# Kernel optimization log

Hardware: AMD Instinct MI355X
Metric: run time of the kernel (lower is better)

Reference implementation:

```python
import jax, jax.numpy as jnp
import numpy as np

B, LQ, LK, E, HID, H = 4, 1024, 2048, 512, 512, 8


def _ln(x, g, b, eps=1e-5):
    mu = jnp.mean(x, -1, keepdims=True)
    var = jnp.mean((x - mu) ** 2, -1, keepdims=True)
    return (x - mu) * jax.lax.rsqrt(var + eps) * g + b


def _mha(q_in, k_in, v_in, Wq, bq, Wk, bk, Wv, bv, Wo, bo, nheads, q_valid, k_valid):
    # torch nn.MultiheadAttention (batch_first, eval/dropout=0) math
    Bq, Lq, Em = q_in.shape
    Lk = k_in.shape[1]
    hd = Em // nheads
    q = (q_in @ Wq.T + bq).reshape(Bq, Lq, nheads, hd)
    k = (k_in @ Wk.T + bk).reshape(Bq, Lk, nheads, hd)
    v = (v_in @ Wv.T + bv).reshape(Bq, Lk, nheads, hd)
    scale = 1.0 / np.sqrt(hd).astype(np.float32)
    s = jnp.einsum('bqhd,bkhd->bhqk', q, k) * scale
    if k_valid is not None:
        # valid query rows may only attend to valid key columns
        s = jnp.where(k_valid[:, None, None, :], s, jnp.finfo(s.dtype).min)
    w = jax.nn.softmax(s, axis=-1)
    # rows beyond a sample's length are fully masked in the torch nested path
    # (softmax -> NaN, later nan_to_num'd to 0); we zero them directly.
    w = jnp.where(q_valid[:, None, :, None], w, 0.0)
    o = jnp.einsum('bhqk,bkhd->bqhd', w, v).reshape(Bq, Lq, Em)
    return o @ Wo.T + bo, jnp.mean(w, axis=1)  # weights averaged over heads


def setup_inputs() -> dict:
    key = jax.random.key(0)
    ks = jax.random.split(key, 32)
    p = lambda i, shape: 0.02 * jax.random.normal(ks[i], shape, dtype=jnp.float32)
    inp = {
        'queries': jax.random.normal(ks[0], (B, LQ, E), dtype=jnp.float32),
        'keys': jax.random.normal(ks[1], (B, LK, E), dtype=jnp.float32),
        'q_len': jax.random.randint(ks[2], (B,), 1, LQ + 1),
        # cross-attention params
        'cWq': p(3, (E, E)), 'cbq': jnp.zeros((E,)),
        'cWk': p(4, (E, E)), 'cbk': jnp.zeros((E,)),
        'cWv': p(5, (E, E)), 'cbv': jnp.zeros((E,)),
        'cWo': p(6, (E, E)), 'cbo': jnp.zeros((E,)),
        # self-attention params
        'sWq': p(7, (HID, HID)), 'sbq': jnp.zeros((HID,)),
        'sWk': p(8, (HID, HID)), 'sbk': jnp.zeros((HID,)),
        'sWv': p(9, (HID, HID)), 'sbv': jnp.zeros((HID,)),
        'sWo': p(10, (HID, HID)), 'sbo': jnp.zeros((HID,)),
        # ffn + norms
        'Wf': p(11, (HID, E)), 'bf': jnp.zeros((HID,)),
        'g_cross': jnp.ones((E,)), 'b_cross': jnp.zeros((E,)),
        'g_ffn': jnp.ones((HID,)), 'b_ffn': jnp.zeros((HID,)),
        'g_self': jnp.ones((HID,)), 'b_self': jnp.zeros((HID,)),
    }
    return inp


def reference(queries, keys, q_len,
              cWq, cbq, cWk, cbk, cWv, cbv, cWo, cbo,
              sWq, sbq, sWk, sbk, sWv, sbv, sWo, sbo,
              Wf, bf, g_cross, b_cross, g_ffn, b_ffn, g_self, b_self):
    valid = jnp.arange(LQ)[None, :] < q_len[:, None]  # [B, LQ] ragged lengths
    q = jnp.where(valid[..., None], queries, 0.0)     # nested -> padded with 0
    # cross attention: valid rows attend to ALL keys (per the nested mask)
    cross, weights = _mha(q, keys, keys, cWq, cbq, cWk, cbk, cWv, cbv, cWo, cbo,
                          H, valid, None)
    q = _ln(jax.nn.silu(cross + q), g_cross, b_cross)
    f = q @ Wf.T + bf
    q = _ln(jax.nn.silu(q + f), g_ffn, b_ffn)  # q_dim == hidden_dim branch
    q = jnp.where(valid[..., None], q, 0.0)    # torch.nan_to_num on padded rows
    # self attention: valid rows attend only to valid rows of the same sample
    so, _ = _mha(q, q, q, sWq, sbq, sWk, sbk, sWv, sbv, sWo, sbo, H, valid, valid)
    q = _ln(jax.nn.silu(q + so), g_self, b_self)
    q = jnp.where(valid[..., None], q, 0.0)    # padded rows discarded by unbind
    return q, weights
```

## Files before the change

kernel.cpp:

```cpp
#include <hip/hip_runtime.h>

#define BB 4
#define SLQ 1024
#define SLK 2048
#define EE 512
#define HH 8
#define HD 64

typedef unsigned short u16;
typedef __attribute__((ext_vector_type(8))) short s16x8;
typedef __attribute__((ext_vector_type(4))) float f32x4;

__device__ __forceinline__ float bf2f(u16 u) {
  union { unsigned int i; float f; } v; v.i = ((unsigned int)u) << 16; return v.f;
}
__device__ __forceinline__ u16 f2bf(float f) {
  union { float f; unsigned int i; } v; v.f = f;
  unsigned int i = v.i;
  return (u16)((i + 0x7fffu + ((i >> 16) & 1u)) >> 16);
}

__device__ __forceinline__ void async16(const u16* g, u16* l) {
  __builtin_amdgcn_global_load_lds(
      (const __attribute__((address_space(1))) unsigned int*)g,
      (__attribute__((address_space(3))) unsigned int*)l, 16, 0, 0);
}

template<int BM, int BN, int MODE, int SKIPQ>
__global__ __launch_bounds__(256, (BM == 128 ? 4 : 6))
void gemm_nt(const u16* __restrict__ A, const u16* __restrict__ Bm,
             const float* __restrict__ bias, u16* __restrict__ C,
             int M, int N, int K, int lda, int ldb, int ldc,
             long sAz, long sBz, long sCz, float alpha, int Lsub,
             const int* __restrict__ qlen)
{
  constexpr int WTM = BM / 2, WTN = BN / 2;
  constexpr int MI = WTM / 16, NI = WTN / 16;
  constexpr int EPAD = WTN + 8;
  constexpr int SM1 = (BM + BN) * 32;
  constexpr int SM2 = (MODE == 0) ? 4 * WTM * EPAD : 0;
  constexpr int SM = (SM1 > SM2) ? SM1 : SM2;

  const int z = blockIdx.z;
  const int tileM = blockIdx.y * BM;
  const int tileN = blockIdx.x * BN;

  if (SKIPQ == 1) { if (tileM >= qlen[z >> 3]) return; }
  if (SKIPQ == 2) { int b = tileM >> 10; if ((tileM & 1023) >= qlen[b]) return; }

  __shared__ __align__(16) u16 smem[SM];
  u16* ldsA = smem;
  u16* ldsB = smem + BM * 32;

  const int t = threadIdx.x;
  const int lane = t & 63;
  const int wave = t >> 6;
  const int waveM = wave >> 1;
  const int waveN = wave & 1;
  const int lm = lane & 15;
  const int kg = lane >> 4;

  const u16* Ab = A + (long)z * sAz + (long)tileM * lda;
  const u16* Bb = Bm + (long)z * sBz + (long)tileN * ldb;

  f32x4 acc[MI][NI];
#pragma unroll
  for (int i = 0; i < MI; ++i)
#pragma unroll
    for (int j = 0; j < NI; ++j) acc[i][j] = (f32x4){0.f, 0.f, 0.f, 0.f};

  for (int kt = 0; kt < K; kt += 32) {
    __syncthreads();
#pragma unroll
    for (int i = 0; i < (BM * 4) / 256; ++i) {
      int c = i * 256 + t;
      async16(Ab + (long)(c >> 2) * lda + kt + (c & 3) * 8, ldsA + (c - lane) * 8);
    }
#pragma unroll
    for (int i = 0; i < (BN * 4) / 256; ++i) {
      int c = i * 256 + t;
      async16(Bb + (long)(c >> 2) * ldb + kt + (c & 3) * 8, ldsB + (c - lane) * 8);
    }
    __syncthreads();

    s16x8 aF[MI], bF[NI];
#pragma unroll
    for (int i = 0; i < MI; ++i)
      aF[i] = *(const s16x8*)&ldsA[(waveM * WTM + i * 16 + lm) * 32 + kg * 8];
#pragma unroll
    for (int j = 0; j < NI; ++j)
      bF[j] = *(const s16x8*)&ldsB[(waveN * WTN + j * 16 + lm) * 32 + kg * 8];
#pragma unroll
    for (int i = 0; i < MI; ++i)
#pragma unroll
      for (int j = 0; j < NI; ++j)
        acc[i][j] = __builtin_amdgcn_mfma_f32_16x16x32_bf16(aF[i], bF[j], acc[i][j], 0, 0, 0);
  }

  if (MODE == 0) {
    u16* ep = smem + wave * (WTM * EPAD);
    __syncthreads();
#pragma unroll
    for (int i = 0; i < MI; ++i)
#pragma unroll
      for (int j = 0; j < NI; ++j) {
        int n = waveN * WTN + j * 16 + lm;
        float bv = bias ? bias[tileN + n] : 0.0f;
#pragma unroll
        for (int r = 0; r < 4; ++r)
          ep[(i * 16 + kg * 4 + r) * EPAD + j * 16 + lm] = f2bf(acc[i][j][r] * alpha + bv);
      }
    const long Crow = (long)z * sCz + (long)(tileM + waveM * WTM) * ldc + tileN + waveN * WTN;
#pragma unroll
    for (int it = 0; it < (WTM * WTN) / 512; ++it) {
      int idx = it * 64 + lane;
      int row = idx / (WTN / 8), seg = idx % (WTN / 8);
      *(uint4*)&C[Crow + (long)row * ldc + seg * 8] =
          *(const uint4*)&ep[row * EPAD + seg * 8];
    }
  } else {
#pragma unroll
    for (int j = 0; j < NI; ++j) {
      int n = tileN + waveN * WTN + j * 16 + lm;
      float bv = bias ? bias[n] : 0.0f;
#pragma unroll
      for (int i = 0; i < MI; ++i) {
#pragma unroll
        for (int r = 0; r < 4; ++r) {
          int m = tileM + waveM * WTM + i * 16 + kg * 4 + r;
          float v = acc[i][j][r] * alpha + bv;
          int b = m / Lsub, l = m - b * Lsub;
          int h = n >> 6, d = n & 63;
          C[(((long)(b * HH + h) * Lsub + l) << 6) + d] = f2bf(v);
        }
      }
    }
  }
}

template<int BM, int BN, int SKIPQ, int NPROJ>
__global__ __launch_bounds__(256, 6)
void gemm_proj(const u16* __restrict__ A,
               const u16* B0, const u16* B1, const u16* B2,
               const float* bias0, const float* bias1, const float* bias2,
               u16* C0, u16* C1, u16* C2,
               int M, int lda, int Lsub, const int* __restrict__ qlen)
{
  constexpr int WTM = BM / 2, WTN = BN / 2;
  constexpr int MI = WTM / 16, NI = WTN / 16;

  const int z = blockIdx.z;
  const int tileM = blockIdx.y * BM;
  const int tileN = blockIdx.x * BN;
  if (SKIPQ == 2) { int b = tileM >> 10; if ((tileM & 1023) >= qlen[b]) return; }

  const u16* Bm = (z == 0) ? B0 : (z == 1) ? B1 : B2;
  const float* bias = (z == 0) ? bias0 : (z == 1) ? bias1 : bias2;
  u16* C = (z == 0) ? C0 : (z == 1) ? C1 : C2;
  const bool tr = (z == NPROJ - 1);

  __shared__ __align__(16) u16 smem[(BM + BN) * 32];
  u16* ldsA = smem;
  u16* ldsB = smem + BM * 32;

  const int t = threadIdx.x;
  const int lane = t & 63;
  const int wave = t >> 6;
  const int waveM = wave >> 1;
  const int waveN = wave & 1;
  const int lm = lane & 15;
  const int kg = lane >> 4;

  const u16* Ab = A + (long)tileM * lda;
  const u16* Bb = Bm + (long)tileN * EE;

  f32x4 acc[MI][NI];
#pragma unroll
  for (int i = 0; i < MI; ++i)
#pragma unroll
    for (int j = 0; j < NI; ++j) acc[i][j] = (f32x4){0.f, 0.f, 0.f, 0.f};

  for (int kt = 0; kt < EE; kt += 32) {
    __syncthreads();
#pragma unroll
    for (int i = 0; i < (BM * 4) / 256; ++i) {
      int c = i * 256 + t;
      async16(Ab + (long)(c >> 2) * lda + kt + (c & 3) * 8, ldsA + (c - lane) * 8);
    }
#pragma unroll
    for (int i = 0; i < (BN * 4) / 256; ++i) {
      int c = i * 256 + t;
      async16(Bb + (long)(c >> 2) * EE + kt + (c & 3) * 8, ldsB + (c - lane) * 8);
    }
    __syncthreads();

    s16x8 aF[MI], bF[NI];
#pragma unroll
    for (int i = 0; i < MI; ++i)
      aF[i] = *(const s16x8*)&ldsA[(waveM * WTM + i * 16 + lm) * 32 + kg * 8];
#pragma unroll
    for (int j = 0; j < NI; ++j)
      bF[j] = *(const s16x8*)&ldsB[(waveN * WTN + j * 16 + lm) * 32 + kg * 8];
#pragma unroll
    for (int i = 0; i < MI; ++i)
#pragma unroll
      for (int j = 0; j < NI; ++j)
        acc[i][j] = __builtin_amdgcn_mfma_f32_16x16x32_bf16(aF[i], bF[j], acc[i][j], 0, 0, 0);
  }

  if (!tr) {
#pragma unroll
    for (int j = 0; j < NI; ++j) {
      int n = tileN + waveN * WTN + j * 16 + lm;
      float bv = bias[n];
#pragma unroll
      for (int i = 0; i < MI; ++i)
#pragma unroll
        for (int r = 0; r < 4; ++r) {
          int m = tileM + waveM * WTM + i * 16 + kg * 4 + r;
          int b = m / Lsub, l = m - b * Lsub;
          int h = n >> 6, d = n & 63;
          C[(((long)(b * HH + h) * Lsub + l) << 6) + d] = f2bf(acc[i][j][r] + bv);
        }
    }
  } else {
    constexpr int PAD = BM + 8;
    const int bb = tileM / Lsub;
    const int l0 = tileM - bb * Lsub;
#pragma unroll
    for (int c = 0; c < BN / 32; ++c) {
      __syncthreads();
#pragma unroll
      for (int j = 0; j < NI; ++j) {
        int nloc = waveN * WTN + j * 16 + lm;
        if (nloc >= c * 32 && nloc < c * 32 + 32) {
          int nl = nloc - c * 32;
          float bv = bias[tileN + nloc];
#pragma unroll
          for (int i = 0; i < MI; ++i)
#pragma unroll
            for (int r = 0; r < 4; ++r) {
              int mm = waveM * WTM + i * 16 + kg * 4 + r;
              smem[nl * PAD + mm] = f2bf(acc[i][j][r] + bv);
            }
        }
      }
      __syncthreads();
#pragma unroll
      for (int v = 0; v < (32 * BM) / (256 * 8); ++v) {
        int idx = v * 256 + t;
        int nl = idx / (BM / 8), m8 = idx % (BM / 8);
        int n = tileN + c * 32 + nl;
        int h = n >> 6, d = n & 63;
        *(uint4*)&C[((long)(bb * HH + h) * HD + d) * Lsub + l0 + m8 * 8] =
            *(const uint4*)&smem[nl * PAD + m8 * 8];
      }
    }
  }
}

__global__ __launch_bounds__(256, 3)
void cross_flash_chunk(const u16* __restrict__ Qc, const u16* __restrict__ Kc,
                       const u16* __restrict__ Vt, u16* __restrict__ Opart,
                       float2* __restrict__ ml, const int* __restrict__ qlen)
{
  const int lin = blockIdx.x;
  const int lid = (lin & 7) * 256 + (lin >> 3);
  const int qt = lid & 15;
  const int bh = (lid >> 4) & 31;
  const int ck = lid >> 9;
  const int b = bh >> 3;
  if (qt * 64 >= qlen[b]) return;

  __shared__ __align__(16) u16 Kt[128 * 72];
  __shared__ __align__(16) u16 Vl[64 * 136];
  __shared__ __align__(16) u16 Pl[4 * 16 * 136];

  const int t = threadIdx.x, lane = t & 63, w = t >> 6;
  const int col = lane & 15, quad = lane >> 4;

  const u16* Qb = Qc + (long)bh * SLQ * HD;
  const u16* Kb = Kc + (long)bh * SLK * HD;
  const u16* Vb = Vt + (long)bh * HD * SLK;

  s16x8 aQ[2];
#pragma unroll
  for (int kk = 0; kk < 2; ++kk)
    aQ[kk] = *(const s16x8*)(Qb + (long)(qt * 64 + w * 16 + col) * HD + kk * 32 + quad * 8);

  f32x4 O[4];
#pragma unroll
  for (int n = 0; n < 4; ++n) O[n] = (f32x4){0.f, 0.f, 0.f, 0.f};
  float mr = -1e30f, lr = 0.f;

  u16* Pw = Pl + w * 16 * 136;

  const int krow = t >> 3, kcol = (t & 7) * 8;
  const int vrow = t >> 4, vcol = (t & 15) * 8;

  uint4 kr0, kr1, kr2, kr3, vr0, vr1, vr2, vr3;
  {
    const int kb = ck * 512;
    kr0 = *(const uint4*)(Kb + (long)(kb + krow) * HD + kcol);
    kr1 = *(const uint4*)(Kb + (long)(kb + krow + 32) * HD + kcol);
    kr2 = *(const uint4*)(Kb + (long)(kb + krow + 64) * HD + kcol);
    kr3 = *(const uint4*)(Kb + (long)(kb + krow + 96) * HD + kcol);
    vr0 = *(const uint4*)(Vb + (long)(vrow) * SLK + kb + vcol);
    vr1 = *(const uint4*)(Vb + (long)(vrow + 16) * SLK + kb + vcol);
    vr2 = *(const uint4*)(Vb + (long)(vrow + 32) * SLK + kb + vcol);
    vr3 = *(const uint4*)(Vb + (long)(vrow + 48) * SLK + kb + vcol);
  }

#pragma unroll
  for (int kt = 0; kt < 4; ++kt) {
    __syncthreads();
    *(uint4*)&Kt[(krow) * 72 + kcol] = kr0;
    *(uint4*)&Kt[(krow + 32) * 72 + kcol] = kr1;
    *(uint4*)&Kt[(krow + 64) * 72 + kcol] = kr2;
    *(uint4*)&Kt[(krow + 96) * 72 + kcol] = kr3;
    *(uint4*)&Vl[(vrow) * 136 + vcol] = vr0;
    *(uint4*)&Vl[(vrow + 16) * 136 + vcol] = vr1;
    *(uint4*)&Vl[(vrow + 32) * 136 + vcol] = vr2;
    *(uint4*)&Vl[(vrow + 48) * 136 + vcol] = vr3;
    if (kt < 3) {
      const int kb = ck * 512 + (kt + 1) * 128;
      kr0 = *(const uint4*)(Kb + (long)(kb + krow) * HD + kcol);
      kr1 = *(const uint4*)(Kb + (long)(kb + krow + 32) * HD + kcol);
      kr2 = *(const uint4*)(Kb + (long)(kb + krow + 64) * HD + kcol);
      kr3 = *(const uint4*)(Kb + (long)(kb + krow + 96) * HD + kcol);
      vr0 = *(const uint4*)(Vb + (long)(vrow) * SLK + kb + vcol);
      vr1 = *(const uint4*)(Vb + (long)(vrow + 16) * SLK + kb + vcol);
      vr2 = *(const uint4*)(Vb + (long)(vrow + 32) * SLK + kb + vcol);
      vr3 = *(const uint4*)(Vb + (long)(vrow + 48) * SLK + kb + vcol);
    }
    __syncthreads();

    f32x4 s[8];
#pragma unroll
    for (int j = 0; j < 8; ++j) s[j] = (f32x4){0.f, 0.f, 0.f, 0.f};
#pragma unroll
    for (int j = 0; j < 8; ++j)
#pragma unroll
      for (int kk = 0; kk < 2; ++kk) {
        s16x8 bK = *(const s16x8*)&Kt[(j * 16 + col) * 72 + kk * 32 + quad * 8];
        s[j] = __builtin_amdgcn_mfma_f32_16x16x32_bf16(bK, aQ[kk], s[j], 0, 0, 0);
      }
#pragma unroll
    for (int j = 0; j < 8; ++j)
#pragma unroll
      for (int r = 0; r < 4; ++r)
        s[j][r] *= 0.125f;

    float tm = s[0][0];
#pragma unroll
    for (int j = 0; j < 8; ++j)
#pragma unroll
      for (int r = 0; r < 4; ++r)
        tm = fmaxf(tm, s[j][r]);
    tm = fmaxf(tm, __shfl_xor(tm, 16));
    tm = fmaxf(tm, __shfl_xor(tm, 32));
    float mnew = fmaxf(mr, tm);
    float alpha = __expf(mr - mnew);
    mr = mnew;
    float ps = 0.f;
#pragma unroll
    for (int j = 0; j < 8; ++j) {
      float p0 = __expf(s[j][0] - mnew);
      float p1 = __expf(s[j][1] - mnew);
      float p2 = __expf(s[j][2] - mnew);
      float p3 = __expf(s[j][3] - mnew);
      ps += (p0 + p1) + (p2 + p3);
      unsigned int lo = (unsigned int)f2bf(p0) | ((unsigned int)f2bf(p1) << 16);
      unsigned int hi = (unsigned int)f2bf(p2) | ((unsigned int)f2bf(p3) << 16);
      *(uint2*)&Pw[col * 136 + j * 16 + quad * 4] = (uint2){lo, hi};
    }
    ps += __shfl_xor(ps, 16);
    ps += __shfl_xor(ps, 32);
    lr = lr * alpha + ps;

    float a0 = __shfl(alpha, quad * 4 + 0);
    float a1 = __shfl(alpha, quad * 4 + 1);
    float a2 = __shfl(alpha, quad * 4 + 2);
    float a3 = __shfl(alpha, quad * 4 + 3);
#pragma unroll
    for (int n = 0; n < 4; ++n) {
      O[n][0] *= a0; O[n][1] *= a1; O[n][2] *= a2; O[n][3] *= a3;
    }
#pragma unroll
    for (int kk = 0; kk < 4; ++kk) {
      s16x8 aP = *(const s16x8*)&Pw[col * 136 + kk * 32 + quad * 8];
#pragma unroll
      for (int n = 0; n < 4; ++n) {
        s16x8 bV = *(const s16x8*)&Vl[(n * 16 + col) * 136 + kk * 32 + quad * 8];
        O[n] = __builtin_amdgcn_mfma_f32_16x16x32_bf16(aP, bV, O[n], 0, 0, 0);
      }
    }
  }

#pragma unroll
  for (int r = 0; r < 4; ++r) {
    int q = qt * 64 + w * 16 + quad * 4 + r;
    long gq = (long)bh * SLQ + q;
#pragma unroll
    for (int n = 0; n < 4; ++n)
      Opart[(gq * 4 + ck) * 64 + n * 16 + col] = f2bf(O[n][r]);
  }
  if (quad == 0) {
    int q = qt * 64 + w * 16 + col;
    ml[((long)bh * SLQ + q) * 4 + ck] = (float2){mr, lr};
  }
}

__global__ __launch_bounds__(256)
void cross_combine(const u16* __restrict__ Opart, const float2* __restrict__ ml,
                   u16* __restrict__ attn, float2* __restrict__ stat,
                   const int* __restrict__ qlen)
{
  int gr = blockIdx.x * 16 + (threadIdx.x >> 4);
  int bh = gr >> 10, q = gr & 1023;
  int b = bh >> 3, h = bh & 7;
  if (q >= qlen[b]) return;
  int d = (threadIdx.x & 15) * 4;
  long base = (long)gr * 4;
  float M = -1e30f;
#pragma unroll
  for (int c = 0; c < 4; ++c) M = fmaxf(M, ml[base + c].x);
  float L = 0.f;
  float ax = 0.f, ay = 0.f, az = 0.f, aw = 0.f;
#pragma unroll
  for (int c = 0; c < 4; ++c) {
    float2 st = ml[base + c];
    float wgt = __expf(st.x - M);
    L += st.y * wgt;
    const u16* p = Opart + (base + c) * 64 + d;
    ax += bf2f(p[0]) * wgt; ay += bf2f(p[1]) * wgt;
    az += bf2f(p[2]) * wgt; aw += bf2f(p[3]) * wgt;
  }
  if (d == 0) stat[gr] = (float2){M, L};
  float inv = 1.0f / L;
  unsigned int lo = (unsigned int)f2bf(ax * inv) | ((unsigned int)f2bf(ay * inv) << 16);
  unsigned int hi = (unsigned int)f2bf(az * inv) | ((unsigned int)f2bf(aw * inv) << 16);
  *(uint2*)&attn[((long)b * SLQ + q) * EE + h * HD + d] = (uint2){lo, hi};
}

__global__ __launch_bounds__(256, 4)
void wmean_recompute(const u16* __restrict__ Qc, const u16* __restrict__ Kc,
                     const float2* __restrict__ stat, float* __restrict__ outw,
                     const int* __restrict__ qlen)
{
  const int kt = blockIdx.x;
  const int qt = blockIdx.y;
  const int b  = blockIdx.z;
  const int qn = qlen[b];
  const int q0 = qt * 64;
  const int t = threadIdx.x, lane = t & 63, w = t >> 6;
  const int col = lane & 15, quad = lane >> 4;

  float* wr = outw + ((long)b * SLQ + q0) * SLK + kt * 128;

  if (q0 >= qn) {
    float4 z = {0.f, 0.f, 0.f, 0.f};
    for (int i = t; i < 64 * 32; i += 256) {
      int row = i >> 5, c = (i & 31) << 2;
      *(float4*)&wr[(long)row * SLK + c] = z;
    }
    return;
  }

  __shared__ __align__(16) u16 Kl[128 * 72];

  const int qw = q0 + w * 16;
  const u16* Kbase = Kc + ((long)b * HH * SLK + (long)kt * 128) * HD;

  const int krow = t >> 3, kcol = (t & 7) * 8;

  uint4 kr0, kr1, kr2, kr3;
  kr0 = *(const uint4*)(Kbase + (long)(krow) * HD + kcol);
  kr1 = *(const uint4*)(Kbase + (long)(krow + 32) * HD + kcol);
  kr2 = *(const uint4*)(Kbase + (long)(krow + 64) * HD + kcol);
  kr3 = *(const uint4*)(Kbase + (long)(krow + 96) * HD + kcol);

  f32x4 acc[8];
#pragma unroll
  for (int j = 0; j < 8; ++j) acc[j] = (f32x4){0.f, 0.f, 0.f, 0.f};

#pragma unroll 1
  for (int h = 0; h < 8; ++h) {
    const int bh = b * 8 + h;
    __syncthreads();
    *(uint4*)&Kl[(krow) * 72 + kcol] = kr0;
    *(uint4*)&Kl[(krow + 32) * 72 + kcol] = kr1;
    *(uint4*)&Kl[(krow + 64) * 72 + kcol] = kr2;
    *(uint4*)&Kl[(krow + 96) * 72 + kcol] = kr3;
    if (h < 7) {
      const u16* Kn = Kbase + (long)(h + 1) * SLK * HD;
      kr0 = *(const uint4*)(Kn + (long)(krow) * HD + kcol);
      kr1 = *(const uint4*)(Kn + (long)(krow + 32) * HD + kcol);
      kr2 = *(const uint4*)(Kn + (long)(krow + 64) * HD + kcol);
      kr3 = *(const uint4*)(Kn + (long)(krow + 96) * HD + kcol);
    }
    const u16* Qb = Qc + ((long)bh * SLQ + qw) * HD;
    s16x8 aQ0 = *(const s16x8*)(Qb + col * HD + quad * 8);
    s16x8 aQ1 = *(const s16x8*)(Qb + col * HD + 32 + quad * 8);
    float m_[4], il_[4];
#pragma unroll
    for (int r = 0; r < 4; ++r) {
      float2 st = stat[(long)bh * SLQ + qw + quad * 4 + r];
      m_[r] = st.x; il_[r] = 0.125f / st.y;
    }
    __syncthreads();

    f32x4 s[8];
#pragma unroll
    for (int j = 0; j < 8; ++j) s[j] = (f32x4){0.f, 0.f, 0.f, 0.f};
#pragma unroll
    for (int j = 0; j < 8; ++j) {
      s16x8 bK0 = *(const s16x8*)&Kl[(j * 16 + col) * 72 + quad * 8];
      s16x8 bK1 = *(const s16x8*)&Kl[(j * 16 + col) * 72 + 32 + quad * 8];
      s[j] = __builtin_amdgcn_mfma_f32_16x16x32_bf16(aQ0, bK0, s[j], 0, 0, 0);
      s[j] = __builtin_amdgcn_mfma_f32_16x16x32_bf16(aQ1, bK1, s[j], 0, 0, 0);
    }
#pragma unroll
    for (int j = 0; j < 8; ++j)
#pragma unroll
      for (int r = 0; r < 4; ++r)
        acc[j][r] += __expf(s[j][r] * 0.125f - m_[r]) * il_[r];
  }

#pragma unroll
  for (int r = 0; r < 4; ++r) {
    int row = w * 16 + quad * 4 + r;
    bool v = (q0 + row) < qn;
#pragma unroll
    for (int j = 0; j < 8; ++j)
      wr[(long)row * SLK + j * 16 + col] = v ? acc[j][r] : 0.f;
  }
}

__global__ __launch_bounds__(256, 3)
void self_flash_chunk(const u16* __restrict__ Qc, const u16* __restrict__ Kc,
                      const u16* __restrict__ Vt, u16* __restrict__ Opart,
                      float2* __restrict__ ml, const int* __restrict__ qlen)
{
  const int lin = blockIdx.x;
  const int lid = (lin & 7) * 256 + (lin >> 3);
  const int qt = lid & 15;
  const int bh = (lid >> 4) & 31;
  const int ck = lid >> 9;
  const int b = bh >> 3;
  const int kmax = qlen[b];
  if (qt * 64 >= kmax || ck * 256 >= kmax) return;

  __shared__ __align__(16) u16 Kt[128 * 72];
  __shared__ __align__(16) u16 Vl[64 * 136];
  __shared__ __align__(16) u16 Pl[4 * 16 * 136];

  const int t = threadIdx.x, lane = t & 63, w = t >> 6;
  const int col = lane & 15, quad = lane >> 4;

  const u16* Qb = Qc + (long)bh * SLQ * HD;
  const u16* Kb = Kc + (long)bh * SLQ * HD;
  const u16* Vb = Vt + (long)bh * HD * SLQ;

  s16x8 aQ[2];
#pragma unroll
  for (int kk = 0; kk < 2; ++kk)
    aQ[kk] = *(const s16x8*)(Qb + (long)(qt * 64 + w * 16 + col) * HD + kk * 32 + quad * 8);

  f32x4 O[4];
#pragma unroll
  for (int n = 0; n < 4; ++n) O[n] = (f32x4){0.f, 0.f, 0.f, 0.f};
  float mr = -1e30f, lr = 0.f;

  u16* Pw = Pl + w * 16 * 136;

  const int krow = t >> 3, kcol = (t & 7) * 8;
  const int vrow = t >> 4, vcol = (t & 15) * 8;

  uint4 kr0, kr1, kr2, kr3, vr0, vr1, vr2, vr3;
  {
    const int kb = ck * 256;
    kr0 = *(const uint4*)(Kb + (long)(kb + krow) * HD + kcol);
    kr1 = *(const uint4*)(Kb + (long)(kb + krow + 32) * HD + kcol);
    kr2 = *(const uint4*)(Kb + (long)(kb + krow + 64) * HD + kcol);
    kr3 = *(const uint4*)(Kb + (long)(kb + krow + 96) * HD + kcol);
    vr0 = *(const uint4*)(Vb + (long)(vrow) * SLQ + kb + vcol);
    vr1 = *(const uint4*)(Vb + (long)(vrow + 16) * SLQ + kb + vcol);
    vr2 = *(const uint4*)(Vb + (long)(vrow + 32) * SLQ + kb + vcol);
    vr3 = *(const uint4*)(Vb + (long)(vrow + 48) * SLQ + kb + vcol);
  }

#pragma unroll
  for (int kt = 0; kt < 2; ++kt) {
    const int k0 = ck * 256 + kt * 128;
    if (k0 >= kmax) break;
    __syncthreads();
    *(uint4*)&Kt[(krow) * 72 + kcol] = kr0;
    *(uint4*)&Kt[(krow + 32) * 72 + kcol] = kr1;
    *(uint4*)&Kt[(krow + 64) * 72 + kcol] = kr2;
    *(uint4*)&Kt[(krow + 96) * 72 + kcol] = kr3;
    *(uint4*)&Vl[(vrow) * 136 + vcol] = vr0;
    *(uint4*)&Vl[(vrow + 16) * 136 + vcol] = vr1;
    *(uint4*)&Vl[(vrow + 32) * 136 + vcol] = vr2;
    *(uint4*)&Vl[(vrow + 48) * 136 + vcol] = vr3;
    if (kt < 1) {
      const int kb = ck * 256 + 128;
      kr0 = *(const uint4*)(Kb + (long)(kb + krow) * HD + kcol);
      kr1 = *(const uint4*)(Kb + (long)(kb + krow + 32) * HD + kcol);
      kr2 = *(const uint4*)(Kb + (long)(kb + krow + 64) * HD + kcol);
      kr3 = *(const uint4*)(Kb + (long)(kb + krow + 96) * HD + kcol);
      vr0 = *(const uint4*)(Vb + (long)(vrow) * SLQ + kb + vcol);
      vr1 = *(const uint4*)(Vb + (long)(vrow + 16) * SLQ + kb + vcol);
      vr2 = *(const uint4*)(Vb + (long)(vrow + 32) * SLQ + kb + vcol);
      vr3 = *(const uint4*)(Vb + (long)(vrow + 48) * SLQ + kb + vcol);
    }
    __syncthreads();

    f32x4 s[8];
#pragma unroll
    for (int j = 0; j < 8; ++j) s[j] = (f32x4){0.f, 0.f, 0.f, 0.f};
#pragma unroll
    for (int j = 0; j < 8; ++j)
#pragma unroll
      for (int kk = 0; kk < 2; ++kk) {
        s16x8 bK = *(const s16x8*)&Kt[(j * 16 + col) * 72 + kk * 32 + quad * 8];
        s[j] = __builtin_amdgcn_mfma_f32_16x16x32_bf16(bK, aQ[kk], s[j], 0, 0, 0);
      }
#pragma unroll
    for (int j = 0; j < 8; ++j)
#pragma unroll
      for (int r = 0; r < 4; ++r) {
        bool ok = (k0 + j * 16 + quad * 4 + r) < kmax;
        s[j][r] = ok ? s[j][r] * 0.125f : -1e30f;
      }

    float tm = s[0][0];
#pragma unroll
    for (int j = 0; j < 8; ++j)
#pragma unroll
      for (int r = 0; r < 4; ++r)
        tm = fmaxf(tm, s[j][r]);
    tm = fmaxf(tm, __shfl_xor(tm, 16));
    tm = fmaxf(tm, __shfl_xor(tm, 32));
    float mnew = fmaxf(mr, tm);
    float alpha = __expf(mr - mnew);
    mr = mnew;
    float ps = 0.f;
#pragma unroll
    for (int j = 0; j < 8; ++j) {
      float p0 = __expf(s[j][0] - mnew);
      float p1 = __expf(s[j][1] - mnew);
      float p2 = __expf(s[j][2] - mnew);
      float p3 = __expf(s[j][3] - mnew);
      ps += (p0 + p1) + (p2 + p3);
      unsigned int lo = (unsigned int)f2bf(p0) | ((unsigned int)f2bf(p1) << 16);
      unsigned int hi = (unsigned int)f2bf(p2) | ((unsigned int)f2bf(p3) << 16);
      *(uint2*)&Pw[col * 136 + j * 16 + quad * 4] = (uint2){lo, hi};
    }
    ps += __shfl_xor(ps, 16);
    ps += __shfl_xor(ps, 32);
    lr = lr * alpha + ps;

    float a0 = __shfl(alpha, quad * 4 + 0);
    float a1 = __shfl(alpha, quad * 4 + 1);
    float a2 = __shfl(alpha, quad * 4 + 2);
    float a3 = __shfl(alpha, quad * 4 + 3);
#pragma unroll
    for (int n = 0; n < 4; ++n) {
      O[n][0] *= a0; O[n][1] *= a1; O[n][2] *= a2; O[n][3] *= a3;
    }
#pragma unroll
    for (int kk = 0; kk < 4; ++kk) {
      s16x8 aP = *(const s16x8*)&Pw[col * 136 + kk * 32 + quad * 8];
#pragma unroll
      for (int n = 0; n < 4; ++n) {
        s16x8 bV = *(const s16x8*)&Vl[(n * 16 + col) * 136 + kk * 32 + quad * 8];
        O[n] = __builtin_amdgcn_mfma_f32_16x16x32_bf16(aP, bV, O[n], 0, 0, 0);
      }
    }
  }

#pragma unroll
  for (int r = 0; r < 4; ++r) {
    int q = qt * 64 + w * 16 + quad * 4 + r;
    long gq = (long)bh * SLQ + q;
#pragma unroll
    for (int n = 0; n < 4; ++n)
      Opart[(gq * 4 + ck) * 64 + n * 16 + col] = f2bf(O[n][r]);
  }
  if (quad == 0) {
    int q = qt * 64 + w * 16 + col;
    ml[((long)bh * SLQ + q) * 4 + ck] = (float2){mr, lr};
  }
}

__global__ __launch_bounds__(256)
void self_combine(const u16* __restrict__ Opart, const float2* __restrict__ ml,
                  u16* __restrict__ attn, const int* __restrict__ qlen)
{
  int gr = blockIdx.x * 16 + (threadIdx.x >> 4);
  int bh = gr >> 10, q = gr & 1023;
  int b = bh >> 3, h = bh & 7;
  int kmax = qlen[b];
  if (q >= kmax) return;
  int NC = (kmax + 255) >> 8;
  int d = (threadIdx.x & 15) * 4;
  long base = (long)gr * 4;
  float M = -1e30f;
  for (int c = 0; c < NC; ++c) M = fmaxf(M, ml[base + c].x);
  float L = 0.f;
  float ax = 0.f, ay = 0.f, az = 0.f, aw = 0.f;
  for (int c = 0; c < NC; ++c) {
    float2 st = ml[base + c];
    float wgt = __expf(st.x - M);
    L += st.y * wgt;
    const u16* p = Opart + (base + c) * 64 + d;
    ax += bf2f(p[0]) * wgt; ay += bf2f(p[1]) * wgt;
    az += bf2f(p[2]) * wgt; aw += bf2f(p[3]) * wgt;
  }
  float inv = 1.0f / L;
  unsigned int lo = (unsigned int)f2bf(ax * inv) | ((unsigned int)f2bf(ay * inv) << 16);
  unsigned int hi = (unsigned int)f2bf(az * inv) | ((unsigned int)f2bf(aw * inv) << 16);
  *(uint2*)&attn[((long)b * SLQ + q) * EE + h * HD + d] = (uint2){lo, hi};
}

__global__ __launch_bounds__(256)
void cvt_all(const float* __restrict__ queries, const float* __restrict__ keys,
             const int* __restrict__ qlen,
             const float* w0, const float* w1, const float* w2, const float* w3,
             const float* w4, const float* w5, const float* w6, const float* w7,
             const float* w8,
             u16* __restrict__ q0, u16* __restrict__ keysb, u16* __restrict__ Wb) {
  int blk = blockIdx.x;
  int t = threadIdx.x;
  const float* src;
  u16* dst;
  long off;
  bool mask = false;
  int b = 0, q = 0;
  if (blk < 1024) {
    off = (long)blk * 2048 + t * 8;
    int row = (int)(off >> 9);
    b = row >> 10; q = row & 1023;
    mask = true;
    src = queries; dst = q0;
  } else if (blk < 3072) {
    off = (long)(blk - 1024) * 2048 + t * 8;
    src = keys; dst = keysb;
  } else {
    int mat = (blk - 3072) >> 7, part = (blk - 3072) & 127;
    const float* srcs[9] = {w0, w1, w2, w3, w4, w5, w6, w7, w8};
    src = srcs[mat];
    off = (long)part * 2048 + t * 8;
    dst = Wb + (long)mat * EE * EE;
  }
  s16x8 o = (s16x8){0, 0, 0, 0, 0, 0, 0, 0};
  if (!mask || q < qlen[b]) {
    float4 a = *(const float4*)&src[off];
    float4 c = *(const float4*)&src[off + 4];
    o[0] = (short)f2bf(a.x); o[1] = (short)f2bf(a.y);
    o[2] = (short)f2bf(a.z); o[3] = (short)f2bf(a.w);
    o[4] = (short)f2bf(c.x); o[5] = (short)f2bf(c.y);
    o[6] = (short)f2bf(c.z); o[7] = (short)f2bf(c.w);
  }
  *(s16x8*)&dst[off] = o;
}

__device__ __forceinline__ float blockSum(float v, float* red4) {
#pragma unroll
  for (int o = 32; o; o >>= 1) v += __shfl_xor(v, o);
  if ((threadIdx.x & 63) == 0) red4[threadIdx.x >> 6] = v;
  __syncthreads();
  v = red4[0] + red4[1] + red4[2] + red4[3];
  __syncthreads();
  return v;
}

template<int OUTF32>
__global__ __launch_bounds__(256)
void silu_ln_kernel(const u16* __restrict__ x1, const u16* __restrict__ x2,
                    const float* __restrict__ g, const float* __restrict__ beta,
                    const int* __restrict__ qlen, void* __restrict__ outv, int mode) {
  int row = blockIdx.x;
  int b = row >> 10, q = row & 1023;
  int t = threadIdx.x;
  if (mode && q >= qlen[b]) {
    if (mode == 1) {
      if (OUTF32) {
        float* o = (float*)outv + (long)row * EE;
        o[2 * t] = 0.f; o[2 * t + 1] = 0.f;
      } else {
        u16* o = (u16*)outv + (long)row * EE;
        *(unsigned int*)&o[2 * t] = 0u;
      }
    }
    return;
  }
  __shared__ float red4[4];
  const u16* p1 = x1 + (long)row * EE;
  const u16* p2 = x2 + (long)row * EE;
  float a0 = bf2f(p1[2 * t]) + bf2f(p2[2 * t]);
  float a1 = bf2f(p1[2 * t + 1]) + bf2f(p2[2 * t + 1]);
  a0 = a0 / (1.f + __expf(-a0));
  a1 = a1 / (1.f + __expf(-a1));
  float mu = blockSum(a0 + a1, red4) * (1.f / 512.f);
  float d0 = a0 - mu, d1 = a1 - mu;
  float var = blockSum(d0 * d0 + d1 * d1, red4) * (1.f / 512.f);
  float rs = rsqrtf(var + 1e-5f);
  float r0 = d0 * rs * g[2 * t] + beta[2 * t];
  float r1 = d1 * rs * g[2 * t + 1] + beta[2 * t + 1];
  if (OUTF32) {
    float* o = (float*)outv + (long)row * EE;
    o[2 * t] = r0; o[2 * t + 1] = r1;
  } else {
    u16* o = (u16*)outv + (long)row * EE;
    o[2 * t] = f2bf(r0); o[2 * t + 1] = f2bf(r1);
  }
}

extern "C" void kernel_launch(void* const* d_in, const int* in_sizes, int n_in,
                              void* d_out, int out_size, void* d_ws, size_t ws_size,
                              hipStream_t stream) {
  const float* queries = (const float*)d_in[0];
  const float* keys    = (const float*)d_in[1];
  const int*   qlen    = (const int*)d_in[2];
  const float* cWq = (const float*)d_in[3],  *cbq = (const float*)d_in[4];
  const float* cWk = (const float*)d_in[5],  *cbk = (const float*)d_in[6];
  const float* cWv = (const float*)d_in[7],  *cbv = (const float*)d_in[8];
  const float* cWo = (const float*)d_in[9],  *cbo = (const float*)d_in[10];
  const float* sWq = (const float*)d_in[11], *sbq = (const float*)d_in[12];
  const float* sWk = (const float*)d_in[13], *sbk = (const float*)d_in[14];
  const float* sWv = (const float*)d_in[15], *sbv = (const float*)d_in[16];
  const float* sWo = (const float*)d_in[17], *sbo = (const float*)d_in[18];
  const float* Wf  = (const float*)d_in[19], *bfb = (const float*)d_in[20];
  const float* g_cross = (const float*)d_in[21], *b_cross = (const float*)d_in[22];
  const float* g_ffn   = (const float*)d_in[23], *b_ffn   = (const float*)d_in[24];
  const float* g_self  = (const float*)d_in[25], *b_self  = (const float*)d_in[26];

  float* out_q = (float*)d_out;
  float* out_w = out_q + (long)BB * SLQ * EE;

  u16* ws = (u16*)d_ws;
  u16* S     = ws;
  u16* Qc    = S   + (long)BB * HH * SLQ * SLK;
  u16* Kc    = Qc  + (long)BB * HH * SLQ * HD;
  u16* Vt    = Kc  + (long)BB * HH * SLK * HD;
  u16* q0    = Vt  + (long)BB * HH * SLK * HD;
  u16* keysb = q0  + (long)BB * SLQ * EE;
  u16* attn  = keysb + (long)BB * SLK * EE;
  u16* proj  = attn + (long)BB * SLQ * EE;
  u16* q1    = proj + (long)BB * SLQ * EE;
  u16* fbuf  = q1  + (long)BB * SLQ * EE;
  u16* q2    = fbuf + (long)BB * SLQ * EE;
  u16* Wb    = q2  + (long)BB * SLQ * EE;
  const long WSLOT = (long)EE * EE;
  u16*    Cpb  = Wb + 9 * WSLOT;
  float2* stat = (float2*)(Cpb + 8388608);

  float2* mlC = (float2*)(S + 33554432);

  u16*    OpS = S;
  float2* mlS = (float2*)(S + 8388608);

  u16* bWq = Wb + 0 * WSLOT; u16* bWk = Wb + 1 * WSLOT; u16* bWv = Wb + 2 * WSLOT;
  u16* bWo = Wb + 3 * WSLOT; u16* bsWq = Wb + 4 * WSLOT; u16* bsWk = Wb + 5 * WSLOT;
  u16* bsWv = Wb + 6 * WSLOT; u16* bsWo = Wb + 7 * WSLOT; u16* bWf = Wb + 8 * WSLOT;

  dim3 blk(256);
  const int MQ = BB * SLQ;
  const int MK = BB * SLK;

  cvt_all<<<dim3(3072 + 9 * 128), blk, 0, stream>>>(
      queries, keys, qlen, cWq, cWk, cWv, cWo, sWq, sWk, sWv, sWo, Wf, q0, keysb, Wb);

  gemm_nt<64, 64, 1, 2><<<dim3(EE / 64, MQ / 64, 1), blk, 0, stream>>>(
      q0, bWq, cbq, Qc, MQ, EE, EE, EE, EE, 0, 0, 0, 0, 1.0f, SLQ, qlen);
  gemm_proj<64, 64, 0, 2><<<dim3(EE / 64, MK / 64, 2), blk, 0, stream>>>(
      keysb, bWk, bWv, nullptr, cbk, cbv, nullptr, Kc, Vt, nullptr, MK, EE, SLK, qlen);

  cross_flash_chunk<<<dim3(2048), blk, 0, stream>>>(Qc, Kc, Vt, Cpb, mlC, qlen);
  cross_combine<<<dim3(2048), blk, 0, stream>>>(Cpb, mlC, attn, stat, qlen);
  wmean_recompute<<<dim3(16, 16, BB), blk, 0, stream>>>(Qc, Kc, stat, out_w, qlen);

  gemm_nt<64, 64, 0, 2><<<dim3(EE / 64, MQ / 64, 1), blk, 0, stream>>>(
      attn, bWo, cbo, proj, MQ, EE, EE, EE, EE, EE, 0, 0, 0, 1.0f, SLQ, qlen);

  silu_ln_kernel<0><<<dim3(MQ), blk, 0, stream>>>(proj, q0, g_cross, b_cross, qlen, q1, 2);

  gemm_nt<64, 64, 0, 2><<<dim3(EE / 64, MQ / 64, 1), blk, 0, stream>>>(
      q1, bWf, bfb, fbuf, MQ, EE, EE, EE, EE, EE, 0, 0, 0, 1.0f, SLQ, qlen);

  silu_ln_kernel<0><<<dim3(MQ), blk, 0, stream>>>(q1, fbuf, g_ffn, b_ffn, qlen, q2, 1);

  gemm_proj<64, 64, 2, 3><<<dim3(EE / 64, MQ / 64, 3), blk, 0, stream>>>(
      q2, bsWq, bsWk, bsWv, sbq, sbk, sbv, Qc, Kc, Vt, MQ, EE, SLQ, qlen);

  self_flash_chunk<<<dim3(2048), blk, 0, stream>>>(Qc, Kc, Vt, OpS, mlS, qlen);
  self_combine<<<dim3(2048), blk, 0, stream>>>(OpS, mlS, attn, qlen);

  gemm_nt<64, 64, 0, 2><<<dim3(EE / 64, MQ / 64, 1), blk, 0, stream>>>(
      attn, bsWo, sbo, proj, MQ, EE, EE, EE, EE, EE, 0, 0, 0, 1.0f, SLQ, qlen);

  silu_ln_kernel<1><<<dim3(MQ), blk, 0, stream>>>(q2, proj, g_self, b_self, qlen, out_q, 1);
}
```

Before: 294.0 us.

## Alias P scratch onto K tile in LDS and raise flash kernel occupancy

Both flash-attention chunk kernels drop their separate P buffer and write softmax probabilities into the K tile's shared memory. A barrier after the QK^T MFMAs keeps that K data from being overwritten while still in use. This cuts LDS per block so the launch bound can move from 3 to 4 blocks per CU, and the row max and sum reductions become tree-shaped for more instruction-level parallelism. The cost is an extra barrier per key tile, and the tighter register budget at 4 blocks per CU may cause spills.

```diff
diff --git a/kernel.cpp b/kernel.cpp
--- a/kernel.cpp
+++ b/kernel.cpp
@@ -259,7 +259,7 @@
   }
 }
 
-__global__ __launch_bounds__(256, 3)
+__global__ __launch_bounds__(256, 4)
 void cross_flash_chunk(const u16* __restrict__ Qc, const u16* __restrict__ Kc,
                        const u16* __restrict__ Vt, u16* __restrict__ Opart,
                        float2* __restrict__ ml, const int* __restrict__ qlen)
@@ -274,7 +274,6 @@
 
   __shared__ __align__(16) u16 Kt[128 * 72];
   __shared__ __align__(16) u16 Vl[64 * 136];
-  __shared__ __align__(16) u16 Pl[4 * 16 * 136];
 
   const int t = threadIdx.x, lane = t & 63, w = t >> 6;
   const int col = lane & 15, quad = lane >> 4;
@@ -293,7 +292,7 @@
   for (int n = 0; n < 4; ++n) O[n] = (f32x4){0.f, 0.f, 0.f, 0.f};
   float mr = -1e30f, lr = 0.f;
 
-  u16* Pw = Pl + w * 16 * 136;
+  u16* Pw = Kt + w * (16 * 136);
 
   const int krow = t >> 3, kcol = (t & 7) * 8;
   const int vrow = t >> 4, vcol = (t & 15) * 8;
@@ -351,29 +350,33 @@
       for (int r = 0; r < 4; ++r)
         s[j][r] *= 0.125f;
 
-    float tm = s[0][0];
+    __syncthreads();
+
+    float mj[8];
 #pragma unroll
     for (int j = 0; j < 8; ++j)
-#pragma unroll
-      for (int r = 0; r < 4; ++r)
-        tm = fmaxf(tm, s[j][r]);
+      mj[j] = fmaxf(fmaxf(s[j][0], s[j][1]), fmaxf(s[j][2], s[j][3]));
+    float tm = fmaxf(fmaxf(fmaxf(mj[0], mj[1]), fmaxf(mj[2], mj[3])),
+                     fmaxf(fmaxf(mj[4], mj[5]), fmaxf(mj[6], mj[7])));
     tm = fmaxf(tm, __shfl_xor(tm, 16));
     tm = fmaxf(tm, __shfl_xor(tm, 32));
     float mnew = fmaxf(mr, tm);
     float alpha = __expf(mr - mnew);
     mr = mnew;
-    float ps = 0.f;
+    float psj[8];
 #pragma unroll
     for (int j = 0; j < 8; ++j) {
       float p0 = __expf(s[j][0] - mnew);
       float p1 = __expf(s[j][1] - mnew);
       float p2 = __expf(s[j][2] - mnew);
       float p3 = __expf(s[j][3] - mnew);
-      ps += (p0 + p1) + (p2 + p3);
+      psj[j] = (p0 + p1) + (p2 + p3);
       unsigned int lo = (unsigned int)f2bf(p0) | ((unsigned int)f2bf(p1) << 16);
       unsigned int hi = (unsigned int)f2bf(p2) | ((unsigned int)f2bf(p3) << 16);
       *(uint2*)&Pw[col * 136 + j * 16 + quad * 4] = (uint2){lo, hi};
     }
+    float ps = ((psj[0] + psj[1]) + (psj[2] + psj[3])) +
+               ((psj[4] + psj[5]) + (psj[6] + psj[7]));
     ps += __shfl_xor(ps, 16);
     ps += __shfl_xor(ps, 32);
     lr = lr * alpha + ps;
@@ -537,7 +540,7 @@
   }
 }
 
-__global__ __launch_bounds__(256, 3)
+__global__ __launch_bounds__(256, 4)
 void self_flash_chunk(const u16* __restrict__ Qc, const u16* __restrict__ Kc,
                       const u16* __restrict__ Vt, u16* __restrict__ Opart,
                       float2* __restrict__ ml, const int* __restrict__ qlen)
@@ -553,7 +556,6 @@
 
   __shared__ __align__(16) u16 Kt[128 * 72];
   __shared__ __align__(16) u16 Vl[64 * 136];
-  __shared__ __align__(16) u16 Pl[4 * 16 * 136];
 
   const int t = threadIdx.x, lane = t & 63, w = t >> 6;
   const int col = lane & 15, quad = lane >> 4;
@@ -572,7 +574,7 @@
   for (int n = 0; n < 4; ++n) O[n] = (f32x4){0.f, 0.f, 0.f, 0.f};
   float mr = -1e30f, lr = 0.f;
 
-  u16* Pw = Pl + w * 16 * 136;
+  u16* Pw = Kt + w * (16 * 136);
 
   const int krow = t >> 3, kcol = (t & 7) * 8;
   const int vrow = t >> 4, vcol = (t & 15) * 8;
@@ -634,29 +636,33 @@
         s[j][r] = ok ? s[j][r] * 0.125f : -1e30f;
       }
 
-    float tm = s[0][0];
+    __syncthreads();
+
+    float mj[8];
 #pragma unroll
     for (int j = 0; j < 8; ++j)
-#pragma unroll
-      for (int r = 0; r < 4; ++r)
-        tm = fmaxf(tm, s[j][r]);
+      mj[j] = fmaxf(fmaxf(s[j][0], s[j][1]), fmaxf(s[j][2], s[j][3]));
+    float tm = fmaxf(fmaxf(fmaxf(mj[0], mj[1]), fmaxf(mj[2], mj[3])),
+                     fmaxf(fmaxf(mj[4], mj[5]), fmaxf(mj[6], mj[7])));
     tm = fmaxf(tm, __shfl_xor(tm, 16));
     tm = fmaxf(tm, __shfl_xor(tm, 32));
     float mnew = fmaxf(mr, tm);
     float alpha = __expf(mr - mnew);
     mr = mnew;
-    float ps = 0.f;
+    float psj[8];
 #pragma unroll
     for (int j = 0; j < 8; ++j) {
       float p0 = __expf(s[j][0] - mnew);
       float p1 = __expf(s[j][1] - mnew);
       float p2 = __expf(s[j][2] - mnew);
       float p3 = __expf(s[j][3] - mnew);
-      ps += (p0 + p1) + (p2 + p3);
+      psj[j] = (p0 + p1) + (p2 + p3);
       unsigned int lo = (unsigned int)f2bf(p0) | ((unsigned int)f2bf(p1) << 16);
       unsigned int hi = (unsigned int)f2bf(p2) | ((unsigned int)f2bf(p3) << 16);
       *(uint2*)&Pw[col * 136 + j * 16 + quad * 4] = (uint2){lo, hi};
     }
+    float ps = ((psj[0] + psj[1]) + (psj[2] + psj[3])) +
+               ((psj[4] + psj[5]) + (psj[6] + psj[7]));
     ps += __shfl_xor(ps, 16);
     ps += __shfl_xor(ps, 32);
     lr = lr * alpha + ps;
```

After: 314.8 us. 7.1% more time.
